# Optimization experiments

Hardware: AMD Instinct MI355X
Metric: run time of the kernel (lower is better)

Reference implementation:

```python
import jax, jax.numpy as jnp
import numpy as np

B, NQ, NV, DIM, HEADS, K = 2, 2048, 2048, 256, 8, 8
HD = DIM // HEADS
HID = 4 * DIM
SCALE = HD ** -0.5
EPS = 1e-5


def setup_inputs() -> dict:
    key = jax.random.key(0)
    ks = jax.random.split(key, 40)
    r = lambda i, s: jax.random.normal(ks[i], s, jnp.float32) * 0.02
    inp = {
        'q': jax.random.normal(ks[0], (B, NQ, DIM), jnp.float32),
        'v': jax.random.normal(ks[1], (B, NV, DIM), jnp.float32),
        'q_pos': jax.random.normal(ks[2], (B, NQ, 3), jnp.float32),
        'v_pos': jax.random.normal(ks[3], (B, NV, 3), jnp.float32),
        'self_knn_index': jax.random.randint(ks[4], (B, NQ, K), 0, NQ, jnp.int32),
        'cross_knn_index': jax.random.randint(ks[5], (B, NQ, K), 0, NV, jnp.int32),
        # LayerNorms (gamma=1, beta=0)
        'norm1_g': jnp.ones(DIM), 'norm1_b': jnp.zeros(DIM),
        'normq_g': jnp.ones(DIM), 'normq_b': jnp.zeros(DIM),
        'normv_g': jnp.ones(DIM), 'normv_b': jnp.zeros(DIM),
        'norm2_g': jnp.ones(DIM), 'norm2_b': jnp.zeros(DIM),
        # self-attention (qkv_bias=False), proj has bias
        'sa_qkv_w': r(6, (DIM, 3 * DIM)),
        'sa_proj_w': r(7, (DIM, DIM)), 'sa_proj_b': jnp.zeros(DIM),
        # cross-attention: q proj and kv proj (no bias), out proj with bias
        'ca_q_w': r(8, (DIM, DIM)),
        'ca_kv_w': r(9, (DIM, 2 * DIM)),
        'ca_proj_w': r(10, (DIM, DIM)), 'ca_proj_b': jnp.zeros(DIM),
        # MLP
        'fc1_w': r(11, (DIM, HID)), 'fc1_b': jnp.zeros(HID),
        'fc2_w': r(12, (HID, DIM)), 'fc2_b': jnp.zeros(DIM),
        # kNN maps
        'knn_w': r(13, (2 * DIM, DIM)), 'knn_b': jnp.zeros(DIM),
        'merge_w': r(14, (2 * DIM, DIM)), 'merge_b': jnp.zeros(DIM),
        'knnx_w': r(15, (2 * DIM, DIM)), 'knnx_b': jnp.zeros(DIM),
        'mergex_w': r(16, (2 * DIM, DIM)), 'mergex_b': jnp.zeros(DIM),
    }
    return inp


def _ln(x, g, b):
    m = x.mean(-1, keepdims=True)
    var = x.var(-1, keepdims=True)
    return (x - m) / jnp.sqrt(var + EPS) * g + b


def _heads(x):  # [B,N,DIM] -> [B,H,N,HD]
    Bx, N, _ = x.shape
    return x.reshape(Bx, N, HEADS, HD).transpose(0, 2, 1, 3)


def _attend(qh, kh, vh, proj_w, proj_b):
    a = jax.nn.softmax(jnp.einsum('bhqd,bhkd->bhqk', qh, kh) * SCALE, axis=-1)
    o = jnp.einsum('bhqk,bhkd->bhqd', a, vh)
    Bx, _, N, _ = o.shape
    o = o.transpose(0, 2, 1, 3).reshape(Bx, N, DIM)
    return o @ proj_w + proj_b


_gather = jax.vmap(lambda pts, idx: pts[idx])  # ([N,D],[Nq,K]) -> [Nq,K,D]


def _knn_feature(qn, vn, idx):  # gather -> diff/cat -> [B,Nq,K,2D]
    local = _gather(vn, idx)                      # [B,Nq,K,D]
    qe = qn[:, :, None, :]                        # [B,Nq,1,D]
    return jnp.concatenate([local - qe, jnp.broadcast_to(qe, local.shape)], -1)


def reference(q, v, q_pos, v_pos, self_knn_index, cross_knn_index,
              norm1_g, norm1_b, normq_g, normq_b, normv_g, normv_b,
              norm2_g, norm2_b, sa_qkv_w, sa_proj_w, sa_proj_b,
              ca_q_w, ca_kv_w, ca_proj_w, ca_proj_b,
              fc1_w, fc1_b, fc2_w, fc2_b,
              knn_w, knn_b, merge_w, merge_b,
              knnx_w, knnx_b, mergex_w, mergex_b):
    # ---- self-attention block with self-kNN branch ----
    nq = _ln(q, norm1_g, norm1_b)
    qkv = nq @ sa_qkv_w
    qh, kh, vh = (_heads(t) for t in jnp.split(qkv, 3, axis=-1))
    sa_out = _attend(qh, kh, vh, sa_proj_w, sa_proj_b)
    f = _knn_feature(nq, nq, self_knn_index)
    knn_out = jax.nn.leaky_relu(f @ knn_w + knn_b, 0.2).max(axis=-2)
    q1 = jnp.concatenate([sa_out, knn_out], -1) @ merge_w + merge_b
    q = q + q1
    # ---- cross-attention block with cross-kNN branch ----
    nq2 = _ln(q, normq_g, normq_b)
    nv = _ln(v, normv_g, normv_b)
    qh = _heads(nq2 @ ca_q_w)
    kh, vh = (_heads(t) for t in jnp.split(nv @ ca_kv_w, 2, axis=-1))
    ca_out = _attend(qh, kh, vh, ca_proj_w, ca_proj_b)
    f = _knn_feature(nq2, nv, cross_knn_index)
    knnx_out = jax.nn.leaky_relu(f @ knnx_w + knnx_b, 0.2).max(axis=-2)
    q2 = jnp.concatenate([ca_out, knnx_out], -1) @ mergex_w + mergex_b
    q = q + q2
    # ---- MLP block ----
    h = _ln(q, norm2_g, norm2_b)
    h = jax.nn.gelu(h @ fc1_w + fc1_b, approximate=False)
    q = q + (h @ fc2_w + fc2_b)
    return q
```

## Files before the change

kernel.cpp:

```cpp
#include <hip/hip_runtime.h>
#include <math.h>

#define NQC   2048
#define NKVC  2048
#define DIMC  256
#define SCALEF 0.17677669529663687f

typedef short bfrag __attribute__((ext_vector_type(8)));
typedef float ffrag __attribute__((ext_vector_type(4)));
typedef unsigned short us8 __attribute__((ext_vector_type(8)));

__device__ __forceinline__ float gelu_exact(float x) {
    return 0.5f * x * (1.0f + erff(x * 0.70710678118654752f));
}
__device__ __forceinline__ unsigned short f2bf(float f) {
    union { float f; unsigned u; } v; v.f = f;
    unsigned r = v.u + 0x7FFFu + ((v.u >> 16) & 1u);
    return (unsigned short)(r >> 16);
}
__device__ __forceinline__ float bf2f(unsigned short u) {
    union { unsigned u; float f; } v; v.u = ((unsigned)u) << 16;
    return v.f;
}

__device__ __forceinline__ void ln_row(
    const float* __restrict__ x, const float* __restrict__ g,
    const float* __restrict__ b, unsigned short* __restrict__ y, int row)
{
    int lane = threadIdx.x & 63;
    const float* xr = x + (size_t)row * DIMC + lane * 4;
    float4 vv = *(const float4*)xr;
    float s  = vv.x + vv.y + vv.z + vv.w;
    float sq = vv.x*vv.x + vv.y*vv.y + vv.z*vv.z + vv.w*vv.w;
    #pragma unroll
    for (int off = 32; off >= 1; off >>= 1) {
        s  += __shfl_xor(s, off);
        sq += __shfl_xor(sq, off);
    }
    float mean = s * (1.0f/DIMC);
    float inv  = rsqrtf(sq * (1.0f/DIMC) - mean*mean + 1e-5f);
    float4 gg = *(const float4*)(g + lane*4);
    float4 bb = *(const float4*)(b + lane*4);
    ushort4 o;
    o.x = f2bf((vv.x - mean) * inv * gg.x + bb.x);
    o.y = f2bf((vv.y - mean) * inv * gg.y + bb.y);
    o.z = f2bf((vv.z - mean) * inv * gg.z + bb.z);
    o.w = f2bf((vv.w - mean) * inv * gg.w + bb.w);
    *(ushort4*)(y + (size_t)row * DIMC + lane * 4) = o;
}

__global__ __launch_bounds__(256) void prep_ln(
    const float* __restrict__ qkv, const float* __restrict__ knn,
    const float* __restrict__ proj, const float* __restrict__ merge,
    const float* __restrict__ caq, const float* __restrict__ knnx,
    const float* __restrict__ cakv, const float* __restrict__ projx,
    const float* __restrict__ mergex, const float* __restrict__ fc1,
    const float* __restrict__ fc2, unsigned short* __restrict__ dst,
    const float* __restrict__ lx, const float* __restrict__ lg,
    const float* __restrict__ lb, unsigned short* __restrict__ ly)
{
    if (blockIdx.x >= 1536) {
        int row = (blockIdx.x - 1536) * 4 + (threadIdx.x >> 6);
        ln_row(lx, lg, lb, ly, row);
        return;
    }
    int e = (blockIdx.x * 256 + threadIdx.x) * 4;
    float v[4];
    float scale = 1.0f;
    if (e < 327680) {
        int n = e >> 8, k = e & 255;
        if (n < 768) {
            const float* s = qkv + (size_t)k * 768 + n;
            #pragma unroll
            for (int i = 0; i < 4; ++i) v[i] = s[(size_t)i * 768];
            if (n < 256) scale = SCALEF;
        } else if (n < 1024) {
            const float* s = knn + (size_t)k * 256 + (n - 768);
            #pragma unroll
            for (int i = 0; i < 4; ++i) v[i] = s[(size_t)i * 256];
        } else {
            const float* s = knn + (size_t)k * 256 + (n - 1024);
            #pragma unroll
            for (int i = 0; i < 4; ++i) v[i] = s[65536 + (size_t)i * 256] - s[(size_t)i * 256];
        }
    } else if (e < 393216) {
        int l = e - 327680, n = l >> 8, k = l & 255;
        const float* s = proj + (size_t)k * 256 + n;
        #pragma unroll
        for (int i = 0; i < 4; ++i) v[i] = s[(size_t)i * 256];
    } else if (e < 524288) {
        int l = e - 393216, n = l >> 9, k = l & 511;
        const float* s = merge + (size_t)k * 256 + n;
        #pragma unroll
        for (int i = 0; i < 4; ++i) v[i] = s[(size_t)i * 256];
    } else if (e < 655360) {
        int l = e - 524288, n = l >> 8, k = l & 255;
        if (n < 256) {
            const float* s = caq + (size_t)k * 256 + n;
            #pragma unroll
            for (int i = 0; i < 4; ++i) v[i] = s[(size_t)i * 256];
            scale = SCALEF;
        } else {
            const float* s = knnx + (size_t)k * 256 + (n - 256);
            #pragma unroll
            for (int i = 0; i < 4; ++i) v[i] = s[65536 + (size_t)i * 256] - s[(size_t)i * 256];
        }
    } else if (e < 851968) {
        int l = e - 655360, n = l >> 8, k = l & 255;
        if (n < 512) {
            const float* s = cakv + (size_t)k * 512 + n;
            #pragma unroll
            for (int i = 0; i < 4; ++i) v[i] = s[(size_t)i * 512];
        } else {
            const float* s = knnx + (size_t)k * 256 + (n - 512);
            #pragma unroll
            for (int i = 0; i < 4; ++i) v[i] = s[(size_t)i * 256];
        }
    } else if (e < 917504) {
        int l = e - 851968, n = l >> 8, k = l & 255;
        const float* s = projx + (size_t)k * 256 + n;
        #pragma unroll
        for (int i = 0; i < 4; ++i) v[i] = s[(size_t)i * 256];
    } else if (e < 1048576) {
        int l = e - 917504, n = l >> 9, k = l & 511;
        const float* s = mergex + (size_t)k * 256 + n;
        #pragma unroll
        for (int i = 0; i < 4; ++i) v[i] = s[(size_t)i * 256];
    } else if (e < 1310720) {
        int l = e - 1048576, n = l >> 8, k = l & 255;
        const float* s = fc1 + (size_t)k * 1024 + n;
        #pragma unroll
        for (int i = 0; i < 4; ++i) v[i] = s[(size_t)i * 1024];
    } else {
        int l = e - 1310720, n = l >> 10, k = l & 1023;
        const float* s = fc2 + (size_t)k * 256 + n;
        #pragma unroll
        for (int i = 0; i < 4; ++i) v[i] = s[(size_t)i * 256];
    }
    ushort4 o;
    o.x = f2bf(v[0] * scale); o.y = f2bf(v[1] * scale);
    o.z = f2bf(v[2] * scale); o.w = f2bf(v[3] * scale);
    *(ushort4*)(dst + e) = o;
}

__global__ __launch_bounds__(256) void ln2_b(
    const float* __restrict__ x1, const float* __restrict__ g1,
    const float* __restrict__ b1, unsigned short* __restrict__ y1,
    const float* __restrict__ x2, const float* __restrict__ g2,
    const float* __restrict__ b2, unsigned short* __restrict__ y2)
{
    int wid = threadIdx.x >> 6;
    int blk = blockIdx.x;
    if (blk < 1024) ln_row(x1, g1, b1, y1, blk * 4 + wid);
    else            ln_row(x2, g2, b2, y2, (blk - 1024) * 4 + wid);
}

__global__ __launch_bounds__(256) void ln_b(
    const float* __restrict__ x, const float* __restrict__ g,
    const float* __restrict__ b, unsigned short* __restrict__ y)
{
    ln_row(x, g, b, y, blockIdx.x * 4 + (threadIdx.x >> 6));
}

template<int ACT, int RESID, int OUTBF>
__global__ __launch_bounds__(256) void gemm64(
    const unsigned short* __restrict__ A, int lda,
    const unsigned short* __restrict__ Wt,
    const float* __restrict__ bias,
    const float* __restrict__ resid, int ldr,
    void* __restrict__ Cp, int ldc, int Kc)
{
    __shared__ unsigned short Alds[64][72];
    __shared__ unsigned short Wlds[64][72];
    const int tid = threadIdx.x;
    const int wid = tid >> 6, lane = tid & 63;
    const int lm = lane & 15, quad = lane >> 4;
    const int wr = wid >> 1, wc = wid & 1;
    const int row0 = blockIdx.y * 64, col0 = blockIdx.x * 64;
    const int ar = tid >> 2, ac = (tid & 3) * 16;
    const unsigned short* Ag = A  + (size_t)(row0 + ar) * lda + ac;
    const unsigned short* Wg = Wt + (size_t)(col0 + ar) * Kc  + ac;

    us8 a0 = *(const us8*)Ag;
    us8 a1 = *(const us8*)(Ag + 8);
    us8 w0 = *(const us8*)Wg;
    us8 w1 = *(const us8*)(Wg + 8);

    ffrag acc[2][2];
    #pragma unroll
    for (int mi = 0; mi < 2; ++mi)
        #pragma unroll
        for (int ni = 0; ni < 2; ++ni)
            acc[mi][ni] = (ffrag){0.f, 0.f, 0.f, 0.f};

    for (int k0 = 0;;) {
        __syncthreads();
        *(us8*)&Alds[ar][ac]   = a0;
        *(us8*)&Alds[ar][ac+8] = a1;
        *(us8*)&Wlds[ar][ac]   = w0;
        *(us8*)&Wlds[ar][ac+8] = w1;
        __syncthreads();
        k0 += 64;
        if (k0 < Kc) {
            a0 = *(const us8*)(Ag + k0);
            a1 = *(const us8*)(Ag + k0 + 8);
            w0 = *(const us8*)(Wg + k0);
            w1 = *(const us8*)(Wg + k0 + 8);
        }
        #pragma unroll
        for (int kc = 0; kc < 2; ++kc) {
            bfrag af[2], bw[2];
            #pragma unroll
            for (int mi = 0; mi < 2; ++mi)
                af[mi] = *(const bfrag*)&Alds[wr*32 + mi*16 + lm][kc*32 + quad*8];
            #pragma unroll
            for (int ni = 0; ni < 2; ++ni)
                bw[ni] = *(const bfrag*)&Wlds[wc*32 + ni*16 + lm][kc*32 + quad*8];
            #pragma unroll
            for (int mi = 0; mi < 2; ++mi)
                #pragma unroll
                for (int ni = 0; ni < 2; ++ni)
                    acc[mi][ni] = __builtin_amdgcn_mfma_f32_16x16x32_bf16(
                        af[mi], bw[ni], acc[mi][ni], 0, 0, 0);
        }
        if (k0 >= Kc) break;
    }
    #pragma unroll
    for (int mi = 0; mi < 2; ++mi) {
        #pragma unroll
        for (int ni = 0; ni < 2; ++ni) {
            int gr = row0 + wr*32 + mi*16 + quad*4;
            int gc = col0 + wc*32 + ni*16 + lm;
            float bv = bias ? bias[gc] : 0.f;
            #pragma unroll
            for (int r = 0; r < 4; ++r) {
                float o = acc[mi][ni][r] + bv;
                if (ACT == 1) o = gelu_exact(o);
                if (RESID) o += resid[(size_t)(gr + r) * ldr + gc];
                if (OUTBF) ((unsigned short*)Cp)[(size_t)(gr + r) * ldc + gc] = f2bf(o);
                else       ((float*)Cp)[(size_t)(gr + r) * ldc + gc] = o;
            }
        }
    }
}

__global__ __launch_bounds__(256) void gemm64_dual(
    const unsigned short* __restrict__ XB,
    const unsigned short* __restrict__ NVB,
    const unsigned short* __restrict__ WT2,
    const unsigned short* __restrict__ WT3,
    unsigned short* __restrict__ A2,
    unsigned short* __restrict__ A3)
{
    const unsigned short* A; const unsigned short* Wt;
    unsigned short* C; int ldc, col0;
    if (blockIdx.x < 8) { A = XB;  Wt = WT2; C = A2; ldc = 512; col0 = blockIdx.x * 64; }
    else                { A = NVB; Wt = WT3; C = A3; ldc = 768; col0 = (blockIdx.x - 8) * 64; }

    __shared__ unsigned short Alds[64][72];
    __shared__ unsigned short Wlds[64][72];
    const int tid = threadIdx.x;
    const int wid = tid >> 6, lane = tid & 63;
    const int lm = lane & 15, quad = lane >> 4;
    const int wr = wid >> 1, wc = wid & 1;
    const int row0 = blockIdx.y * 64;
    const int ar = tid >> 2, ac = (tid & 3) * 16;
    const unsigned short* Ag = A  + (size_t)(row0 + ar) * 256 + ac;
    const unsigned short* Wg = Wt + (size_t)(col0 + ar) * 256 + ac;

    us8 a0 = *(const us8*)Ag;
    us8 a1 = *(const us8*)(Ag + 8);
    us8 w0 = *(const us8*)Wg;
    us8 w1 = *(const us8*)(Wg + 8);

    ffrag acc[2][2];
    #pragma unroll
    for (int mi = 0; mi < 2; ++mi)
        #pragma unroll
        for (int ni = 0; ni < 2; ++ni)
            acc[mi][ni] = (ffrag){0.f, 0.f, 0.f, 0.f};

    for (int k0 = 0;;) {
        __syncthreads();
        *(us8*)&Alds[ar][ac]   = a0;
        *(us8*)&Alds[ar][ac+8] = a1;
        *(us8*)&Wlds[ar][ac]   = w0;
        *(us8*)&Wlds[ar][ac+8] = w1;
        __syncthreads();
        k0 += 64;
        if (k0 < 256) {
            a0 = *(const us8*)(Ag + k0);
            a1 = *(const us8*)(Ag + k0 + 8);
            w0 = *(const us8*)(Wg + k0);
            w1 = *(const us8*)(Wg + k0 + 8);
        }
        #pragma unroll
        for (int kc = 0; kc < 2; ++kc) {
            bfrag af[2], bw[2];
            #pragma unroll
            for (int mi = 0; mi < 2; ++mi)
                af[mi] = *(const bfrag*)&Alds[wr*32 + mi*16 + lm][kc*32 + quad*8];
            #pragma unroll
            for (int ni = 0; ni < 2; ++ni)
                bw[ni] = *(const bfrag*)&Wlds[wc*32 + ni*16 + lm][kc*32 + quad*8];
            #pragma unroll
            for (int mi = 0; mi < 2; ++mi)
                #pragma unroll
                for (int ni = 0; ni < 2; ++ni)
                    acc[mi][ni] = __builtin_amdgcn_mfma_f32_16x16x32_bf16(
                        af[mi], bw[ni], acc[mi][ni], 0, 0, 0);
        }
        if (k0 >= 256) break;
    }
    #pragma unroll
    for (int mi = 0; mi < 2; ++mi) {
        #pragma unroll
        for (int ni = 0; ni < 2; ++ni) {
            int gr = row0 + wr*32 + mi*16 + quad*4;
            int gc = col0 + wc*32 + ni*16 + lm;
            #pragma unroll
            for (int r = 0; r < 4; ++r)
                C[(size_t)(gr + r) * ldc + gc] = f2bf(acc[mi][ni][r]);
        }
    }
}

__global__ __launch_bounds__(256) void gemm64_comb(
    const unsigned short* __restrict__ Op, const float* __restrict__ Lp,
    const unsigned short* __restrict__ Wt,
    const float* __restrict__ bias,
    unsigned short* __restrict__ C, int ldc)
{
    __shared__ unsigned short Alds[64][72];
    __shared__ unsigned short Wlds[64][72];
    const int tid = threadIdx.x;
    const int wid = tid >> 6, lane = tid & 63;
    const int lm = lane & 15, quad = lane >> 4;
    const int wr = wid >> 1, wc = wid & 1;
    const int row0 = blockIdx.y * 64, col0 = blockIdx.x * 64;
    const int ar = tid >> 2, ac = (tid & 3) * 16;
    const int grow = row0 + ar;
    const unsigned short* O0 = Op + (size_t)grow * 256 + ac;
    const unsigned short* O1 = Op + (size_t)(4096 + grow) * 256 + ac;
    const float* L0 = Lp + (size_t)grow * 8;
    const float* L1 = Lp + (size_t)(4096 + grow) * 8;
    const unsigned short* Wg = Wt + (size_t)(col0 + ar) * 256 + ac;

    us8 o00 = *(const us8*)O0;
    us8 o01 = *(const us8*)(O0 + 8);
    us8 o10 = *(const us8*)O1;
    us8 o11 = *(const us8*)(O1 + 8);
    float li = 1.0f / (L0[ac >> 5] + L1[ac >> 5]);
    us8 w0 = *(const us8*)Wg;
    us8 w1 = *(const us8*)(Wg + 8);

    ffrag acc[2][2];
    #pragma unroll
    for (int mi = 0; mi < 2; ++mi)
        #pragma unroll
        for (int ni = 0; ni < 2; ++ni)
            acc[mi][ni] = (ffrag){0.f, 0.f, 0.f, 0.f};

    for (int k0 = 0;;) {
        us8 ac0, ac1;
        #pragma unroll
        for (int i = 0; i < 8; ++i) {
            ac0[i] = f2bf((bf2f(o00[i]) + bf2f(o10[i])) * li);
            ac1[i] = f2bf((bf2f(o01[i]) + bf2f(o11[i])) * li);
        }
        __syncthreads();
        *(us8*)&Alds[ar][ac]   = ac0;
        *(us8*)&Alds[ar][ac+8] = ac1;
        *(us8*)&Wlds[ar][ac]   = w0;
        *(us8*)&Wlds[ar][ac+8] = w1;
        __syncthreads();
        k0 += 64;
        if (k0 < 256) {
            o00 = *(const us8*)(O0 + k0);
            o01 = *(const us8*)(O0 + k0 + 8);
            o10 = *(const us8*)(O1 + k0);
            o11 = *(const us8*)(O1 + k0 + 8);
            li = 1.0f / (L0[(k0 + ac) >> 5] + L1[(k0 + ac) >> 5]);
            w0 = *(const us8*)(Wg + k0);
            w1 = *(const us8*)(Wg + k0 + 8);
        }
        #pragma unroll
        for (int kc = 0; kc < 2; ++kc) {
            bfrag af[2], bw[2];
            #pragma unroll
            for (int mi = 0; mi < 2; ++mi)
                af[mi] = *(const bfrag*)&Alds[wr*32 + mi*16 + lm][kc*32 + quad*8];
            #pragma unroll
            for (int ni = 0; ni < 2; ++ni)
                bw[ni] = *(const bfrag*)&Wlds[wc*32 + ni*16 + lm][kc*32 + quad*8];
            #pragma unroll
            for (int mi = 0; mi < 2; ++mi)
                #pragma unroll
                for (int ni = 0; ni < 2; ++ni)
                    acc[mi][ni] = __builtin_amdgcn_mfma_f32_16x16x32_bf16(
                        af[mi], bw[ni], acc[mi][ni], 0, 0, 0);
        }
        if (k0 >= 256) break;
    }
    #pragma unroll
    for (int mi = 0; mi < 2; ++mi) {
        #pragma unroll
        for (int ni = 0; ni < 2; ++ni) {
            int gr = row0 + wr*32 + mi*16 + quad*4;
            int gc = col0 + wc*32 + ni*16 + lm;
            float bv = bias[gc];
            #pragma unroll
            for (int r = 0; r < 4; ++r)
                C[(size_t)(gr + r) * ldc + gc] = f2bf(acc[mi][ni][r] + bv);
        }
    }
}

__global__ __launch_bounds__(256) void attn_gather(
    const unsigned short* __restrict__ Qp, int ldq,
    const unsigned short* __restrict__ Kp, int ldk,
    const unsigned short* __restrict__ Vp, int ldv,
    unsigned short* __restrict__ Op, float* __restrict__ Lp,
    const unsigned short* __restrict__ P, int ldp,
    const unsigned short* __restrict__ Base, int ldb,
    const float* __restrict__ gbias, const int* __restrict__ idx,
    unsigned short* __restrict__ gout, int ldgo)
{
    __shared__ unsigned short Klds[64][40];
    __shared__ unsigned short Vt[32][72];
    __shared__ unsigned short Plds[4][16][72];
    int tid = threadIdx.x, wid = tid >> 6, lane = tid & 63;

    if (blockIdx.z >= 4) {
        int gbid = blockIdx.x + 32 * (blockIdx.y + 8 * (blockIdx.z - 4));
        int q = gbid * 4 + wid;
        int b = q >> 11;
        int c = lane * 4;
        ushort4 bu = *(const ushort4*)(Base + (size_t)q * ldb + c);
        float4 bi = *(const float4*)(gbias + c);
        float bsx = bf2f(bu.x) + bi.x, bsy = bf2f(bu.y) + bi.y;
        float bsz = bf2f(bu.z) + bi.z, bsw = bf2f(bu.w) + bi.w;
        float4 acc = make_float4(-3e38f, -3e38f, -3e38f, -3e38f);
        const int* ip = idx + (size_t)q * 8;
        #pragma unroll
        for (int k = 0; k < 8; ++k) {
            int j = ip[k];
            ushort4 pu = *(const ushort4*)(P + ((size_t)(b * NKVC + j)) * ldp + c);
            float t;
            t = bsx + bf2f(pu.x); t = t > 0.f ? t : 0.2f * t; acc.x = fmaxf(acc.x, t);
            t = bsy + bf2f(pu.y); t = t > 0.f ? t : 0.2f * t; acc.y = fmaxf(acc.y, t);
            t = bsz + bf2f(pu.z); t = t > 0.f ? t : 0.2f * t; acc.z = fmaxf(acc.z, t);
            t = bsw + bf2f(pu.w); t = t > 0.f ? t : 0.2f * t; acc.w = fmaxf(acc.w, t);
        }
        ushort4 o;
        o.x = f2bf(acc.x); o.y = f2bf(acc.y); o.z = f2bf(acc.z); o.w = f2bf(acc.w);
        *(ushort4*)(gout + (size_t)q * ldgo + c) = o;
        return;
    }

    int zc = blockIdx.z, bb = zc >> 1, ck = zc & 1;
    int h = blockIdx.y;
    int hoff = h * 32;
    int lm = lane & 15, quad = lane >> 4;
    size_t qbase  = (size_t)bb * NQC;
    size_t kvbase = (size_t)bb * NKVC;
    int q0 = blockIdx.x * 64 + wid * 16;

    bfrag aq = *(const bfrag*)(Qp + (qbase + q0 + lm) * (size_t)ldq + hoff + quad * 8);

    float l_r[4] = {0.f, 0.f, 0.f, 0.f};
    ffrag oacc[2];
    oacc[0] = (ffrag){0.f, 0.f, 0.f, 0.f};
    oacc[1] = (ffrag){0.f, 0.f, 0.f, 0.f};

    const int kkey = tid >> 2, kd0 = (tid & 3) * 8;
    const int vkey = tid & 63, vd0 = (tid >> 6) * 8;
    const unsigned short* kg0 = Kp + (kvbase + kkey) * (size_t)ldk + hoff + kd0;
    const unsigned short* vg0 = Vp + (kvbase + vkey) * (size_t)ldv + hoff + vd0;

    for (int kt = ck * 16; kt < ck * 16 + 16; ++kt) {
        us8 kv = *(const us8*)(kg0 + (size_t)kt * 64 * ldk);
        us8 vv = *(const us8*)(vg0 + (size_t)kt * 64 * ldv);
        __syncthreads();
        *(us8*)&Klds[kkey][kd0] = kv;
        #pragma unroll
        for (int i = 0; i < 8; ++i) Vt[vd0 + i][vkey] = vv[i];
        __syncthreads();

        ffrag sacc[4];
        #pragma unroll
        for (int t = 0; t < 4; ++t) {
            bfrag bk = *(const bfrag*)&Klds[t*16 + lm][quad * 8];
            sacc[t] = __builtin_amdgcn_mfma_f32_16x16x32_bf16(
                aq, bk, (ffrag){0.f,0.f,0.f,0.f}, 0, 0, 0);
        }

        #pragma unroll
        for (int r = 0; r < 4; ++r) {
            float p0 = __expf(sacc[0][r]), p1 = __expf(sacc[1][r]);
            float p2 = __expf(sacc[2][r]), p3 = __expf(sacc[3][r]);
            l_r[r] += (p0 + p1) + (p2 + p3);
            int row = quad * 4 + r;
            Plds[wid][row][lm +  0] = f2bf(p0);
            Plds[wid][row][lm + 16] = f2bf(p1);
            Plds[wid][row][lm + 32] = f2bf(p2);
            Plds[wid][row][lm + 48] = f2bf(p3);
        }
        asm volatile("s_waitcnt lgkmcnt(0)" ::: "memory");

        #pragma unroll
        for (int kc = 0; kc < 2; ++kc) {
            bfrag ap = *(const bfrag*)&Plds[wid][lm][kc*32 + quad*8];
            #pragma unroll
            for (int nt = 0; nt < 2; ++nt) {
                bfrag bv = *(const bfrag*)&Vt[nt*16 + lm][kc*32 + quad*8];
                oacc[nt] = __builtin_amdgcn_mfma_f32_16x16x32_bf16(
                    ap, bv, oacc[nt], 0, 0, 0);
            }
        }
    }
    #pragma unroll
    for (int nt = 0; nt < 2; ++nt)
        #pragma unroll
        for (int r = 0; r < 4; ++r)
            Op[((size_t)ck * 4096 + qbase + q0 + quad*4 + r) * 256 + hoff + nt*16 + lm]
                = f2bf(oacc[nt][r]);
    #pragma unroll
    for (int r = 0; r < 4; ++r) {
        float l = l_r[r];
        l += __shfl_xor(l, 1);
        l += __shfl_xor(l, 2);
        l += __shfl_xor(l, 4);
        l += __shfl_xor(l, 8);
        if (lm == 0)
            Lp[((size_t)ck * 4096 + qbase + q0 + quad*4 + r) * 8 + h] = l;
    }
}

extern "C" void kernel_launch(void* const* d_in, const int* in_sizes, int n_in,
                              void* d_out, int out_size, void* d_ws, size_t ws_size,
                              hipStream_t stream) {
    const float* q_in   = (const float*)d_in[0];
    const float* v_in   = (const float*)d_in[1];
    const int*   idx_s  = (const int*)d_in[4];
    const int*   idx_x  = (const int*)d_in[5];
    const float* n1g = (const float*)d_in[6],  *n1b = (const float*)d_in[7];
    const float* nqg = (const float*)d_in[8],  *nqb = (const float*)d_in[9];
    const float* nvg = (const float*)d_in[10], *nvb = (const float*)d_in[11];
    const float* n2g = (const float*)d_in[12], *n2b = (const float*)d_in[13];
    const float* sa_qkv_w  = (const float*)d_in[14];
    const float* sa_proj_w = (const float*)d_in[15];
    const float* sa_proj_b = (const float*)d_in[16];
    const float* ca_q_w    = (const float*)d_in[17];
    const float* ca_kv_w   = (const float*)d_in[18];
    const float* ca_proj_w = (const float*)d_in[19];
    const float* ca_proj_b = (const float*)d_in[20];
    const float* fc1_w = (const float*)d_in[21], *fc1_b = (const float*)d_in[22];
    const float* fc2_w = (const float*)d_in[23], *fc2_b = (const float*)d_in[24];
    const float* knn_w   = (const float*)d_in[25], *knn_b   = (const float*)d_in[26];
    const float* merge_w = (const float*)d_in[27], *merge_b = (const float*)d_in[28];
    const float* knnx_w  = (const float*)d_in[29], *knnx_b  = (const float*)d_in[30];
    const float* mergex_w = (const float*)d_in[31], *mergex_b = (const float*)d_in[32];
    float* out = (float*)d_out;

    unsigned short* A1      = (unsigned short*)d_ws;
    unsigned short* A2      = A1;
    unsigned short* A3      = A1 + (size_t)4096 * 512;
    unsigned short* Hb      = A1;
    unsigned short* CC      = A1 + (size_t)4096 * 1280;
    unsigned short* XB      = CC + (size_t)4096 * 512;
    unsigned short* NVB     = XB + (size_t)4096 * 256;
    unsigned short* WT      = NVB + (size_t)4096 * 256;
    unsigned short* WT1     = WT;
    unsigned short* WTproj  = WT + 327680;
    unsigned short* WTmerge = WT + 393216;
    unsigned short* WT2     = WT + 524288;
    unsigned short* WT3     = WT + 655360;
    unsigned short* WTprojx = WT + 851968;
    unsigned short* WTmergex= WT + 917504;
    unsigned short* WTfc1   = WT + 1048576;
    unsigned short* WTfc2   = WT + 1310720;
    unsigned short* Opart   = WT + 1572864;
    float* Lpart = (float*)(Opart + (size_t)2 * 4096 * 256);

    dim3 blk(256);
    dim3 gAG(NQC / 64, 8, 8);

    prep_ln<<<dim3(2560), blk, 0, stream>>>(sa_qkv_w, knn_w, sa_proj_w, merge_w,
        ca_q_w, knnx_w, ca_kv_w, ca_proj_w, mergex_w, fc1_w, fc2_w, WT,
        q_in, n1g, n1b, XB);

    gemm64<0,0,1><<<dim3(20,64), blk, 0, stream>>>(XB, 256, WT1,
        nullptr, nullptr, 0, A1, 1280, 256);
    attn_gather<<<gAG, blk, 0, stream>>>(A1, 1280, A1+256, 1280, A1+512, 1280,
        Opart, Lpart, A1+768, 1280, A1+1024, 1280, knn_b, idx_s, CC+256, 512);
    gemm64_comb<<<dim3(4,64), blk, 0, stream>>>(Opart, Lpart, WTproj,
        sa_proj_b, CC, 512);
    gemm64<0,1,0><<<dim3(4,64), blk, 0, stream>>>(CC, 512, WTmerge,
        merge_b, q_in, 256, out, 256, 512);

    ln2_b<<<dim3(2048), blk, 0, stream>>>(out, nqg, nqb, XB,
        v_in, nvg, nvb, NVB);
    gemm64_dual<<<dim3(20,64), blk, 0, stream>>>(XB, NVB, WT2, WT3, A2, A3);
    attn_gather<<<gAG, blk, 0, stream>>>(A2, 512, A3, 768, A3+256, 768,
        Opart, Lpart, A3+512, 768, A2+256, 512, knnx_b, idx_x, CC+256, 512);
    gemm64_comb<<<dim3(4,64), blk, 0, stream>>>(Opart, Lpart, WTprojx,
        ca_proj_b, CC, 512);
    gemm64<0,1,0><<<dim3(4,64), blk, 0, stream>>>(CC, 512, WTmergex,
        mergex_b, out, 256, out, 256, 512);

    ln_b<<<dim3(1024), blk, 0, stream>>>(out, n2g, n2b, XB);
    gemm64<1,0,1><<<dim3(16,64), blk, 0, stream>>>(XB, 256, WTfc1,
        fc1_b, nullptr, 0, Hb, 1024, 256);
    gemm64<0,1,0><<<dim3(4,64), blk, 0, stream>>>(Hb, 1024, WTfc2,
        fc2_b, out, 256, out, 256, 1024);
}
```

Measured before the change: 261.4 us.

## Fold attention output projection into merge weights and fuse comb+merge GEMMs

Precomputes proj_w @ merge_w[:256] (and the matching bias terms) inside the weight prep kernel, so the attention output projection and the merge GEMM collapse into a single GEMM over the concatenation of the combined attention partials and the kNN features. This removes one GEMM launch and the intermediate bf16 CC buffer round trip for both the self-attention and cross-attention blocks. In exchange, the prep kernel gains fp32 SIMT matmul blocks and a bias-folding reduction, and the fused weights are rounded to bf16 after the product, which slightly changes numerics.

Result: slower. 267.2 us (+2.2%).

```diff
diff --git a/kernel.cpp b/kernel.cpp
--- a/kernel.cpp
+++ b/kernel.cpp
@@ -57,16 +57,81 @@
     const float* __restrict__ mergex, const float* __restrict__ fc1,
     const float* __restrict__ fc2, unsigned short* __restrict__ dst,
     const float* __restrict__ lx, const float* __restrict__ lg,
-    const float* __restrict__ lb, unsigned short* __restrict__ ly)
-{
-    if (blockIdx.x >= 1536) {
-        int row = (blockIdx.x - 1536) * 4 + (threadIdx.x >> 6);
+    const float* __restrict__ lb, unsigned short* __restrict__ ly,
+    const float* __restrict__ pb, const float* __restrict__ mb,
+    const float* __restrict__ pbx, const float* __restrict__ mbx,
+    float* __restrict__ biasN)
+{
+    __shared__ float As[16][64];
+    __shared__ float Bs[16][64];
+    int bx = blockIdx.x;
+    if (bx >= 2592) {
+        __shared__ float red[4];
+        int bb = bx - 2592;
+        int z = bb >> 8, n = bb & 255;
+        const float* PB = z ? pbx : pb;
+        const float* MW = z ? mergex : merge;
+        const float* MB = z ? mbx : mb;
+        int k = threadIdx.x;
+        float s = PB[k] * MW[(size_t)k * 256 + n];
+        #pragma unroll
+        for (int off = 32; off >= 1; off >>= 1) s += __shfl_xor(s, off);
+        int wid = threadIdx.x >> 6;
+        if ((threadIdx.x & 63) == 0) red[wid] = s;
+        __syncthreads();
+        if (threadIdx.x == 0)
+            biasN[z * 256 + n] = MB[n] + red[0] + red[1] + red[2] + red[3];
+        return;
+    }
+    if (bx >= 2560) {
+        int bb = bx - 2560;
+        int fx = bb & 3, fy = (bb >> 2) & 3, fz = bb >> 4;
+        const float* A = fz ? projx : proj;
+        const float* B = fz ? mergex : merge;
+        unsigned short* D = dst + (fz ? 917504 : 393216);
+        int tid = threadIdx.x;
+        int tx = tid & 15, ty = tid >> 4;
+        int row0 = fy * 64, col0 = fx * 64;
+        int arow = tid >> 2, acol = (tid & 3) * 4;
+        int brow = tid >> 4, bcol = (tid & 15) * 4;
+        float acc[4][4] = {};
+        for (int j0 = 0; j0 < 256; j0 += 16) {
+            __syncthreads();
+            float4 av = *(const float4*)(A + (size_t)(row0 + arow) * 256 + j0 + acol);
+            float4 bv = *(const float4*)(B + (size_t)(j0 + brow) * 256 + col0 + bcol);
+            As[acol+0][arow] = av.x; As[acol+1][arow] = av.y;
+            As[acol+2][arow] = av.z; As[acol+3][arow] = av.w;
+            *(float4*)&Bs[brow][bcol] = bv;
+            __syncthreads();
+            #pragma unroll
+            for (int j = 0; j < 16; ++j) {
+                float4 a4 = *(const float4*)&As[j][ty*4];
+                float4 b4 = *(const float4*)&Bs[j][tx*4];
+                float ar[4] = {a4.x, a4.y, a4.z, a4.w};
+                float br[4] = {b4.x, b4.y, b4.z, b4.w};
+                #pragma unroll
+                for (int ii = 0; ii < 4; ++ii)
+                    #pragma unroll
+                    for (int jj = 0; jj < 4; ++jj)
+                        acc[ii][jj] = fmaf(ar[ii], br[jj], acc[ii][jj]);
+            }
+        }
+        #pragma unroll
+        for (int ii = 0; ii < 4; ++ii)
+            #pragma unroll
+            for (int jj = 0; jj < 4; ++jj)
+                D[(size_t)(col0 + tx*4 + jj) * 512 + row0 + ty*4 + ii] = f2bf(acc[ii][jj]);
+        return;
+    }
+    if (bx >= 1536) {
+        int row = (bx - 1536) * 4 + (threadIdx.x >> 6);
         ln_row(lx, lg, lb, ly, row);
         return;
     }
-    int e = (blockIdx.x * 256 + threadIdx.x) * 4;
+    int e = (bx * 256 + threadIdx.x) * 4;
     float v[4];
     float scale = 1.0f;
+    bool skip = false;
     if (e < 327680) {
         int n = e >> 8, k = e & 255;
         if (n < 768) {
@@ -90,9 +155,12 @@
         for (int i = 0; i < 4; ++i) v[i] = s[(size_t)i * 256];
     } else if (e < 524288) {
         int l = e - 393216, n = l >> 9, k = l & 511;
-        const float* s = merge + (size_t)k * 256 + n;
-        #pragma unroll
-        for (int i = 0; i < 4; ++i) v[i] = s[(size_t)i * 256];
+        if (k < 256) { skip = true; v[0]=v[1]=v[2]=v[3]=0.f; }
+        else {
+            const float* s = merge + (size_t)k * 256 + n;
+            #pragma unroll
+            for (int i = 0; i < 4; ++i) v[i] = s[(size_t)i * 256];
+        }
     } else if (e < 655360) {
         int l = e - 524288, n = l >> 8, k = l & 255;
         if (n < 256) {
@@ -123,9 +191,12 @@
         for (int i = 0; i < 4; ++i) v[i] = s[(size_t)i * 256];
     } else if (e < 1048576) {
         int l = e - 917504, n = l >> 9, k = l & 511;
-        const float* s = mergex + (size_t)k * 256 + n;
-        #pragma unroll
-        for (int i = 0; i < 4; ++i) v[i] = s[(size_t)i * 256];
+        if (k < 256) { skip = true; v[0]=v[1]=v[2]=v[3]=0.f; }
+        else {
+            const float* s = mergex + (size_t)k * 256 + n;
+            #pragma unroll
+            for (int i = 0; i < 4; ++i) v[i] = s[(size_t)i * 256];
+        }
     } else if (e < 1310720) {
         int l = e - 1048576, n = l >> 8, k = l & 255;
         const float* s = fc1 + (size_t)k * 1024 + n;
@@ -137,10 +208,12 @@
         #pragma unroll
         for (int i = 0; i < 4; ++i) v[i] = s[(size_t)i * 256];
     }
-    ushort4 o;
-    o.x = f2bf(v[0] * scale); o.y = f2bf(v[1] * scale);
-    o.z = f2bf(v[2] * scale); o.w = f2bf(v[3] * scale);
-    *(ushort4*)(dst + e) = o;
+    if (!skip) {
+        ushort4 o;
+        o.x = f2bf(v[0] * scale); o.y = f2bf(v[1] * scale);
+        o.z = f2bf(v[2] * scale); o.w = f2bf(v[3] * scale);
+        *(ushort4*)(dst + e) = o;
+    }
 }
 
 __global__ __launch_bounds__(256) void ln2_b(
@@ -325,11 +398,13 @@
     }
 }
 
-__global__ __launch_bounds__(256) void gemm64_comb(
+__global__ __launch_bounds__(256) void gemm64_mc(
     const unsigned short* __restrict__ Op, const float* __restrict__ Lp,
+    const unsigned short* __restrict__ Kn,
     const unsigned short* __restrict__ Wt,
-    const float* __restrict__ bias,
-    unsigned short* __restrict__ C, int ldc)
+    const float* __restrict__ biasN,
+    const float* __restrict__ resid,
+    float* __restrict__ Cp)
 {
     __shared__ unsigned short Alds[64][72];
     __shared__ unsigned short Wlds[64][72];
@@ -340,19 +415,33 @@
     const int row0 = blockIdx.y * 64, col0 = blockIdx.x * 64;
     const int ar = tid >> 2, ac = (tid & 3) * 16;
     const int grow = row0 + ar;
-    const unsigned short* O0 = Op + (size_t)grow * 256 + ac;
-    const unsigned short* O1 = Op + (size_t)(4096 + grow) * 256 + ac;
+    const unsigned short* O0 = Op + (size_t)grow * 256;
+    const unsigned short* O1 = O0 + (size_t)4096 * 256;
     const float* L0 = Lp + (size_t)grow * 8;
-    const float* L1 = Lp + (size_t)(4096 + grow) * 8;
-    const unsigned short* Wg = Wt + (size_t)(col0 + ar) * 256 + ac;
-
-    us8 o00 = *(const us8*)O0;
-    us8 o01 = *(const us8*)(O0 + 8);
-    us8 o10 = *(const us8*)O1;
-    us8 o11 = *(const us8*)(O1 + 8);
-    float li = 1.0f / (L0[ac >> 5] + L1[ac >> 5]);
-    us8 w0 = *(const us8*)Wg;
-    us8 w1 = *(const us8*)(Wg + 8);
+    const float* L1 = L0 + (size_t)4096 * 8;
+    const unsigned short* Kr = Kn + (size_t)grow * 256;
+    const unsigned short* Wg = Wt + (size_t)(col0 + ar) * 512;
+
+    us8 a0, a1, w0, w1;
+    auto load_a = [&](int k0, us8& x0, us8& x1) {
+        if (k0 < 256) {
+            int kk = k0 + ac, hh = kk >> 5;
+            float li = 1.0f / (L0[hh] + L1[hh]);
+            us8 p00 = *(const us8*)(O0 + kk), p01 = *(const us8*)(O0 + kk + 8);
+            us8 p10 = *(const us8*)(O1 + kk), p11 = *(const us8*)(O1 + kk + 8);
+            #pragma unroll
+            for (int i = 0; i < 8; ++i) {
+                x0[i] = f2bf((bf2f(p00[i]) + bf2f(p10[i])) * li);
+                x1[i] = f2bf((bf2f(p01[i]) + bf2f(p11[i])) * li);
+            }
+        } else {
+            x0 = *(const us8*)(Kr + k0 - 256 + ac);
+            x1 = *(const us8*)(Kr + k0 - 256 + ac + 8);
+        }
+    };
+    load_a(0, a0, a1);
+    w0 = *(const us8*)(Wg + ac);
+    w1 = *(const us8*)(Wg + ac + 8);
 
     ffrag acc[2][2];
     #pragma unroll
@@ -362,27 +451,17 @@
             acc[mi][ni] = (ffrag){0.f, 0.f, 0.f, 0.f};
 
     for (int k0 = 0;;) {
-        us8 ac0, ac1;
-        #pragma unroll
-        for (int i = 0; i < 8; ++i) {
-            ac0[i] = f2bf((bf2f(o00[i]) + bf2f(o10[i])) * li);
-            ac1[i] = f2bf((bf2f(o01[i]) + bf2f(o11[i])) * li);
-        }
-        __syncthreads();
-        *(us8*)&Alds[ar][ac]   = ac0;
-        *(us8*)&Alds[ar][ac+8] = ac1;
+        __syncthreads();
+        *(us8*)&Alds[ar][ac]   = a0;
+        *(us8*)&Alds[ar][ac+8] = a1;
         *(us8*)&Wlds[ar][ac]   = w0;
         *(us8*)&Wlds[ar][ac+8] = w1;
         __syncthreads();
         k0 += 64;
-        if (k0 < 256) {
-            o00 = *(const us8*)(O0 + k0);
-            o01 = *(const us8*)(O0 + k0 + 8);
-            o10 = *(const us8*)(O1 + k0);
-            o11 = *(const us8*)(O1 + k0 + 8);
-            li = 1.0f / (L0[(k0 + ac) >> 5] + L1[(k0 + ac) >> 5]);
-            w0 = *(const us8*)(Wg + k0);
-            w1 = *(const us8*)(Wg + k0 + 8);
+        if (k0 < 512) {
+            load_a(k0, a0, a1);
+            w0 = *(const us8*)(Wg + k0 + ac);
+            w1 = *(const us8*)(Wg + k0 + ac + 8);
         }
         #pragma unroll
         for (int kc = 0; kc < 2; ++kc) {
@@ -400,7 +479,7 @@
                     acc[mi][ni] = __builtin_amdgcn_mfma_f32_16x16x32_bf16(
                         af[mi], bw[ni], acc[mi][ni], 0, 0, 0);
         }
-        if (k0 >= 256) break;
+        if (k0 >= 512) break;
     }
     #pragma unroll
     for (int mi = 0; mi < 2; ++mi) {
@@ -408,10 +487,12 @@
         for (int ni = 0; ni < 2; ++ni) {
             int gr = row0 + wr*32 + mi*16 + quad*4;
             int gc = col0 + wc*32 + ni*16 + lm;
-            float bv = bias[gc];
-            #pragma unroll
-            for (int r = 0; r < 4; ++r)
-                C[(size_t)(gr + r) * ldc + gc] = f2bf(acc[mi][ni][r] + bv);
+            float bv = biasN[gc];
+            #pragma unroll
+            for (int r = 0; r < 4; ++r) {
+                float o = acc[mi][ni][r] + bv + resid[(size_t)(gr + r) * 256 + gc];
+                Cp[(size_t)(gr + r) * 256 + gc] = o;
+            }
         }
     }
 }
@@ -567,47 +648,43 @@
     unsigned short* A2      = A1;
     unsigned short* A3      = A1 + (size_t)4096 * 512;
     unsigned short* Hb      = A1;
-    unsigned short* CC      = A1 + (size_t)4096 * 1280;
-    unsigned short* XB      = CC + (size_t)4096 * 512;
+    unsigned short* KN      = A1 + (size_t)4096 * 1280;
+    unsigned short* XB      = KN + (size_t)4096 * 256;
     unsigned short* NVB     = XB + (size_t)4096 * 256;
     unsigned short* WT      = NVB + (size_t)4096 * 256;
     unsigned short* WT1     = WT;
-    unsigned short* WTproj  = WT + 327680;
     unsigned short* WTmerge = WT + 393216;
     unsigned short* WT2     = WT + 524288;
     unsigned short* WT3     = WT + 655360;
-    unsigned short* WTprojx = WT + 851968;
     unsigned short* WTmergex= WT + 917504;
     unsigned short* WTfc1   = WT + 1048576;
     unsigned short* WTfc2   = WT + 1310720;
     unsigned short* Opart   = WT + 1572864;
     float* Lpart = (float*)(Opart + (size_t)2 * 4096 * 256);
+    float* biasN = Lpart + (size_t)2 * 4096 * 8;
 
     dim3 blk(256);
     dim3 gAG(NQC / 64, 8, 8);
 
-    prep_ln<<<dim3(2560), blk, 0, stream>>>(sa_qkv_w, knn_w, sa_proj_w, merge_w,
+    prep_ln<<<dim3(3104), blk, 0, stream>>>(sa_qkv_w, knn_w, sa_proj_w, merge_w,
         ca_q_w, knnx_w, ca_kv_w, ca_proj_w, mergex_w, fc1_w, fc2_w, WT,
-        q_in, n1g, n1b, XB);
+        q_in, n1g, n1b, XB,
+        sa_proj_b, merge_b, ca_proj_b, mergex_b, biasN);
 
     gemm64<0,0,1><<<dim3(20,64), blk, 0, stream>>>(XB, 256, WT1,
         nullptr, nullptr, 0, A1, 1280, 256);
     attn_gather<<<gAG, blk, 0, stream>>>(A1, 1280, A1+256, 1280, A1+512, 1280,
-        Opart, Lpart, A1+768, 1280, A1+1024, 1280, knn_b, idx_s, CC+256, 512);
-    gemm64_comb<<<dim3(4,64), blk, 0, stream>>>(Opart, Lpart, WTproj,
-        sa_proj_b, CC, 512);
-    gemm64<0,1,0><<<dim3(4,64), blk, 0, stream>>>(CC, 512, WTmerge,
-        merge_b, q_in, 256, out, 256, 512);
+        Opart, Lpart, A1+768, 1280, A1+1024, 1280, knn_b, idx_s, KN, 256);
+    gemm64_mc<<<dim3(4,64), blk, 0, stream>>>(Opart, Lpart, KN, WTmerge,
+        biasN, q_in, out);
 
     ln2_b<<<dim3(2048), blk, 0, stream>>>(out, nqg, nqb, XB,
         v_in, nvg, nvb, NVB);
     gemm64_dual<<<dim3(20,64), blk, 0, stream>>>(XB, NVB, WT2, WT3, A2, A3);
     attn_gather<<<gAG, blk, 0, stream>>>(A2, 512, A3, 768, A3+256, 768,
-        Opart, Lpart, A3+512, 768, A2+256, 512, knnx_b, idx_x, CC+256, 512);
-    gemm64_comb<<<dim3(4,64), blk, 0, stream>>>(Opart, Lpart, WTprojx,
-        ca_proj_b, CC, 512);
-    gemm64<0,1,0><<<dim3(4,64), blk, 0, stream>>>(CC, 512, WTmergex,
-        mergex_b, out, 256, out, 256, 512);
+        Opart, Lpart, A3+512, 768, A2+256, 512, knnx_b, idx_x, KN, 256);
+    gemm64_mc<<<dim3(4,64), blk, 0, stream>>>(Opart, Lpart, KN, WTmergex,
+        biasN + 256, out, out);
 
     ln_b<<<dim3(1024), blk, 0, stream>>>(out, n2g, n2b, XB);
     gemm64<1,0,1><<<dim3(16,64), blk, 0, stream>>>(XB, 256, WTfc1,
```

## Split K across two wave groups in narrow-output GEMMs with LDS reduction

Applied to the files above, without the earlier changes.

Adds a 512-thread GEMM variant in which two groups of four waves each handle half of the K dimension for the same 64x64 output tile, then combine partial sums through shared memory before the bias/residual epilogue. It replaces the merge, mergex and fc2 GEMMs, which launch only 256 blocks for a 256-wide output and a long K. The goal is more waves per tile and a shorter serial K loop on an under-filled GPU. In exchange it uses more LDS per block (the Red buffer and doubled tiles) and adds extra barriers and a reduction step. An unused KN alias is also added.

Result: no change. 258.5 us (-1.1%).

```diff
diff --git a/kernel.cpp b/kernel.cpp
--- a/kernel.cpp
+++ b/kernel.cpp
@@ -239,6 +239,110 @@
                 if (RESID) o += resid[(size_t)(gr + r) * ldr + gc];
                 if (OUTBF) ((unsigned short*)Cp)[(size_t)(gr + r) * ldc + gc] = f2bf(o);
                 else       ((float*)Cp)[(size_t)(gr + r) * ldc + gc] = o;
+            }
+        }
+    }
+}
+
+template<int ACT, int RESID, int OUTBF>
+__global__ __launch_bounds__(512) void gemm64x8(
+    const unsigned short* __restrict__ A, int lda,
+    const unsigned short* __restrict__ Wt,
+    const float* __restrict__ bias,
+    const float* __restrict__ resid, int ldr,
+    void* __restrict__ Cp, int ldc, int Kc)
+{
+    __shared__ unsigned short Alds[2][64][72];
+    __shared__ unsigned short Wlds[2][64][72];
+    __shared__ float Red[64][68];
+    const int tid = threadIdx.x;
+    const int g = tid >> 8;
+    const int t = tid & 255;
+    const int wid2 = (tid >> 6) & 3, lane = tid & 63;
+    const int lm = lane & 15, quad = lane >> 4;
+    const int wr = wid2 >> 1, wc = wid2 & 1;
+    const int row0 = blockIdx.y * 64, col0 = blockIdx.x * 64;
+    const int ar = t >> 2, ac = (t & 3) * 16;
+    const int KH = Kc >> 1;
+    const unsigned short* Ag = A  + (size_t)(row0 + ar) * lda + g * KH + ac;
+    const unsigned short* Wg = Wt + (size_t)(col0 + ar) * Kc  + g * KH + ac;
+
+    us8 a0 = *(const us8*)Ag;
+    us8 a1 = *(const us8*)(Ag + 8);
+    us8 w0 = *(const us8*)Wg;
+    us8 w1 = *(const us8*)(Wg + 8);
+
+    ffrag acc[2][2];
+    #pragma unroll
+    for (int mi = 0; mi < 2; ++mi)
+        #pragma unroll
+        for (int ni = 0; ni < 2; ++ni)
+            acc[mi][ni] = (ffrag){0.f, 0.f, 0.f, 0.f};
+
+    for (int k0 = 0;;) {
+        __syncthreads();
+        *(us8*)&Alds[g][ar][ac]   = a0;
+        *(us8*)&Alds[g][ar][ac+8] = a1;
+        *(us8*)&Wlds[g][ar][ac]   = w0;
+        *(us8*)&Wlds[g][ar][ac+8] = w1;
+        __syncthreads();
+        k0 += 64;
+        if (k0 < KH) {
+            a0 = *(const us8*)(Ag + k0);
+            a1 = *(const us8*)(Ag + k0 + 8);
+            w0 = *(const us8*)(Wg + k0);
+            w1 = *(const us8*)(Wg + k0 + 8);
+        }
+        #pragma unroll
+        for (int kc = 0; kc < 2; ++kc) {
+            bfrag af[2], bw[2];
+            #pragma unroll
+            for (int mi = 0; mi < 2; ++mi)
+                af[mi] = *(const bfrag*)&Alds[g][wr*32 + mi*16 + lm][kc*32 + quad*8];
+            #pragma unroll
+            for (int ni = 0; ni < 2; ++ni)
+                bw[ni] = *(const bfrag*)&Wlds[g][wc*32 + ni*16 + lm][kc*32 + quad*8];
+            #pragma unroll
+            for (int mi = 0; mi < 2; ++mi)
+                #pragma unroll
+                for (int ni = 0; ni < 2; ++ni)
+                    acc[mi][ni] = __builtin_amdgcn_mfma_f32_16x16x32_bf16(
+                        af[mi], bw[ni], acc[mi][ni], 0, 0, 0);
+        }
+        if (k0 >= KH) break;
+    }
+    __syncthreads();
+    if (g == 1) {
+        #pragma unroll
+        for (int mi = 0; mi < 2; ++mi)
+            #pragma unroll
+            for (int ni = 0; ni < 2; ++ni) {
+                int lr = wr*32 + mi*16 + quad*4;
+                int lc = wc*32 + ni*16 + lm;
+                #pragma unroll
+                for (int r = 0; r < 4; ++r)
+                    Red[lr + r][lc] = acc[mi][ni][r];
+            }
+    }
+    __syncthreads();
+    if (g == 0) {
+        #pragma unroll
+        for (int mi = 0; mi < 2; ++mi) {
+            #pragma unroll
+            for (int ni = 0; ni < 2; ++ni) {
+                int lr = wr*32 + mi*16 + quad*4;
+                int lc = wc*32 + ni*16 + lm;
+                int gr = row0 + lr;
+                int gc = col0 + lc;
+                float bv = bias ? bias[gc] : 0.f;
+                #pragma unroll
+                for (int r = 0; r < 4; ++r) {
+                    float o = acc[mi][ni][r] + Red[lr + r][lc] + bv;
+                    if (ACT == 1) o = gelu_exact(o);
+                    if (RESID) o += resid[(size_t)(gr + r) * ldr + gc];
+                    if (OUTBF) ((unsigned short*)Cp)[(size_t)(gr + r) * ldc + gc] = f2bf(o);
+                    else       ((float*)Cp)[(size_t)(gr + r) * ldc + gc] = o;
+                }
             }
         }
     }
@@ -567,7 +671,8 @@
     unsigned short* A2      = A1;
     unsigned short* A3      = A1 + (size_t)4096 * 512;
     unsigned short* Hb      = A1;
-    unsigned short* CC      = A1 + (size_t)4096 * 1280;
+    unsigned short* KN      = A1 + (size_t)4096 * 1280;
+    unsigned short* CC      = KN;
     unsigned short* XB      = CC + (size_t)4096 * 512;
     unsigned short* NVB     = XB + (size_t)4096 * 256;
     unsigned short* WT      = NVB + (size_t)4096 * 256;
@@ -583,7 +688,7 @@
     unsigned short* Opart   = WT + 1572864;
     float* Lpart = (float*)(Opart + (size_t)2 * 4096 * 256);
 
-    dim3 blk(256);
+    dim3 blk(256), blk8(512);
     dim3 gAG(NQC / 64, 8, 8);
 
     prep_ln<<<dim3(2560), blk, 0, stream>>>(sa_qkv_w, knn_w, sa_proj_w, merge_w,
@@ -596,7 +701,7 @@
         Opart, Lpart, A1+768, 1280, A1+1024, 1280, knn_b, idx_s, CC+256, 512);
     gemm64_comb<<<dim3(4,64), blk, 0, stream>>>(Opart, Lpart, WTproj,
         sa_proj_b, CC, 512);
-    gemm64<0,1,0><<<dim3(4,64), blk, 0, stream>>>(CC, 512, WTmerge,
+    gemm64x8<0,1,0><<<dim3(4,64), blk8, 0, stream>>>(CC, 512, WTmerge,
         merge_b, q_in, 256, out, 256, 512);
 
     ln2_b<<<dim3(2048), blk, 0, stream>>>(out, nqg, nqb, XB,
@@ -606,12 +711,12 @@
         Opart, Lpart, A3+512, 768, A2+256, 512, knnx_b, idx_x, CC+256, 512);
     gemm64_comb<<<dim3(4,64), blk, 0, stream>>>(Opart, Lpart, WTprojx,
         ca_proj_b, CC, 512);
-    gemm64<0,1,0><<<dim3(4,64), blk, 0, stream>>>(CC, 512, WTmergex,
+    gemm64x8<0,1,0><<<dim3(4,64), blk8, 0, stream>>>(CC, 512, WTmergex,
         mergex_b, out, 256, out, 256, 512);
 
     ln_b<<<dim3(1024), blk, 0, stream>>>(out, n2g, n2b, XB);
     gemm64<1,0,1><<<dim3(16,64), blk, 0, stream>>>(XB, 256, WTfc1,
         fc1_b, nullptr, 0, Hb, 1024, 256);
-    gemm64<0,1,0><<<dim3(4,64), blk, 0, stream>>>(Hb, 1024, WTfc2,
+    gemm64x8<0,1,0><<<dim3(4,64), blk8, 0, stream>>>(Hb, 1024, WTfc2,
         fc2_b, out, 256, out, 256, 1024);
 }
```
